# Kernel optimization log

Measured on AMD Instinct MI355X. Metric: run time of the kernel, lower is better.

The kernel has to match this reference:

```python
import jax, jax.numpy as jnp
import numpy as np

H = 8  # hidden size (hardcoded in the module)


def _lstm_scan(x, Wih, Whh, b):
    """Unidirectional LSTM over x:[B,T,I] with PyTorch gate order (i,f,g,o).
    Wih:[4H,I], Whh:[4H,H], b:[4H] (= b_ih + b_hh). Returns h seq [B,T,H]."""
    B = x.shape[0]
    # Precompute input projections for all timesteps in one GEMM: [T,B,4H]
    xg = jnp.einsum('bti,gi->tbg', x, Wih) + b

    def step(carry, xt):
        h, c = carry
        z = xt + h @ Whh.T
        i, f, g, o = jnp.split(z, 4, axis=-1)
        c = jax.nn.sigmoid(f) * c + jax.nn.sigmoid(i) * jnp.tanh(g)
        h = jax.nn.sigmoid(o) * jnp.tanh(c)
        return (h, c), h

    init = (jnp.zeros((B, H), x.dtype), jnp.zeros((B, H), x.dtype))
    _, hs = jax.lax.scan(step, init, xg)  # hs: [T,B,H]
    return jnp.swapaxes(hs, 0, 1)


def _bilstm(x, Wih_f, Whh_f, b_f, Wih_b, Whh_b, b_b):
    fwd = _lstm_scan(x, Wih_f, Whh_f, b_f)
    bwd = _lstm_scan(x[:, ::-1], Wih_b, Whh_b, b_b)[:, ::-1]
    return jnp.concatenate([fwd, bwd], axis=-1)  # [B,T,2H]


def setup_inputs() -> dict:
    key = jax.random.key(0)
    ks = jax.random.split(key, 17)
    s = 1.0 / np.sqrt(H)  # PyTorch uniform(-1/sqrt(H), 1/sqrt(H)) init

    def u(k, shape):
        return jax.random.uniform(k, shape, jnp.float32, -s, s)

    x = jax.random.normal(ks[0], (256, 4096, 8), jnp.float32)
    inp = {'x': x}
    # LSTM params: biases are b_ih + b_hh fused (mathematically identical)
    names = [('Wih1f', (4 * H, 8)), ('Whh1f', (4 * H, H)), ('b1f', (4 * H,)),
             ('Wih1b', (4 * H, 8)), ('Whh1b', (4 * H, H)), ('b1b', (4 * H,)),
             ('Wih2f', (4 * H, 8)), ('Whh2f', (4 * H, H)), ('b2f', (4 * H,)),
             ('Wih2b', (4 * H, 8)), ('Whh2b', (4 * H, H)), ('b2b', (4 * H,)),
             ('W1', (8, 2 * H)), ('bl1', (8,)),
             ('W2', (8, 2 * H)), ('bl2', (8,))]
    for i, (name, shape) in enumerate(names):
        inp[name] = u(ks[i + 1], shape)
    return inp


def reference(x, Wih1f, Whh1f, b1f, Wih1b, Whh1b, b1b,
              Wih2f, Whh2f, b2f, Wih2b, Whh2b, b2b,
              W1, bl1, W2, bl2):
    h1 = _bilstm(x, Wih1f, Whh1f, b1f, Wih1b, Whh1b, b1b)   # [B,T,16]
    y1 = h1 @ W1.T + bl1                                     # [B,T,8]
    h2 = _bilstm(y1, Wih2f, Whh2f, b2f, Wih2b, Whh2b, b2b)  # [B,T,16]
    return h2 @ W2.T + bl2                                   # [B,T,8]
```

## Files before the change

kernel.cpp:

```cpp
#include <hip/hip_runtime.h>

#define T_LEN 4096
#define B_SZ  256

typedef float v2f __attribute__((ext_vector_type(2)));
typedef float v4f __attribute__((ext_vector_type(4)));

__device__ __forceinline__ float fexp2(float x) { return __builtin_amdgcn_exp2f(x); }
__device__ __forceinline__ float frcp(float x)  { return __builtin_amdgcn_rcpf(x); }

template<int S>
__device__ __forceinline__ float rorN(float v) {
    return __int_as_float(__builtin_amdgcn_update_dpp(
        0, __float_as_int(v), 0x120 + S, 0xf, 0xf, true));
}

template<int OFF>
__device__ __forceinline__ v4f aload(const float* p) {
    v4f r;
    asm volatile("global_load_dwordx4 %0, %1, off offset:%2"
                 : "=v"(r) : "v"(p), "i"(OFF) : "memory");
    return r;
}
__device__ __forceinline__ void aatomic(float* p, float v) {
    asm volatile("global_atomic_add_f32 %0, %1, off"
                 :: "v"(p), "v"(v) : "memory");
}

__global__ void init_bias_kernel(const float* __restrict__ bl1,
                                 const float* __restrict__ bl2,
                                 float* __restrict__ y1,
                                 float* __restrict__ out)
{
    const long idx = (long)blockIdx.x * blockDim.x + threadIdx.x;
    float4 a1 = make_float4(bl1[0], bl1[1], bl1[2], bl1[3]);
    float4 b1 = make_float4(bl1[4], bl1[5], bl1[6], bl1[7]);
    float4 a2 = make_float4(bl2[0], bl2[1], bl2[2], bl2[3]);
    float4 b2 = make_float4(bl2[4], bl2[5], bl2[6], bl2[7]);
    float4* y4 = (float4*)y1;
    float4* o4 = (float4*)out;
    y4[idx * 2 + 0] = a1;
    y4[idx * 2 + 1] = b1;
    o4[idx * 2 + 0] = a2;
    o4[idx * 2 + 1] = b2;
}

template<int ST>
__device__ __forceinline__ void rec_body(
    const float* x,
    const float* Wih,
    const float* Whh,
    const float* bias,
    const float* Wp,
    int dcol,
    float* y,
    int b0)
{
    const int tid  = threadIdx.x;
    const int cl   = tid & 15;
    const int j    = cl & 7;
    const int half = cl >> 3;
    const int b    = b0 + (tid >> 4);

    const int rA = half * 16 + j;
    const int rB = half * 16 + 8 + j;

    const float NL2E = -1.4426950408889634f;
    const float GSC  = 2.0f * NL2E;
    const float sA   = half ? GSC : NL2E;
    const float sB   = NL2E;
    const float aselA = half ? 2.0f : 1.0f;
    const float bselA = half ? -1.0f : 0.0f;

    v2f Whk[8], Wik[8];
    float Wcp[8];
    #pragma unroll
    for (int s = 0; s < 8; ++s) {
        const int k = (j - s) & 7;
        Whk[s] = (v2f){Whh[rA * 8 + k] * sA, Whh[rB * 8 + k] * sB};
        Wcp[s] = Wp[j * 16 + dcol + k] * 0.5f;
    }
    #pragma unroll
    for (int k = 0; k < 8; ++k)
        Wik[k] = (v2f){Wih[rA * 8 + k] * sA, Wih[rB * 8 + k] * sB};
    const v2f bpk = (v2f){bias[rA] * sA, bias[rB] * sB};

    const int start = (ST > 0) ? 0 : (T_LEN - 1);
    const float* xp = x + ((long)b * T_LEN + start) * 8;
    float*       wp = y + ((long)b * T_LEN + start) * 8 + j;

    float c = 0.0f, h = 0.0f;

    auto step = [&](v4f xa, v4f xb, bool doProj) {
        v2f ip = bpk;
        ip = __builtin_elementwise_fma(Wik[0], (v2f){xa.x, xa.x}, ip);
        ip = __builtin_elementwise_fma(Wik[1], (v2f){xa.y, xa.y}, ip);
        ip = __builtin_elementwise_fma(Wik[2], (v2f){xa.z, xa.z}, ip);
        ip = __builtin_elementwise_fma(Wik[3], (v2f){xa.w, xa.w}, ip);
        ip = __builtin_elementwise_fma(Wik[4], (v2f){xb.x, xb.x}, ip);
        ip = __builtin_elementwise_fma(Wik[5], (v2f){xb.y, xb.y}, ip);
        ip = __builtin_elementwise_fma(Wik[6], (v2f){xb.z, xb.z}, ip);
        ip = __builtin_elementwise_fma(Wik[7], (v2f){xb.w, xb.w}, ip);

        float hr0 = h;
        float hr1 = rorN<1>(h);
        float hr2 = rorN<2>(h);
        float hr3 = rorN<3>(h);
        float hr4 = rorN<4>(h);
        float hr5 = rorN<5>(h);
        float hr6 = rorN<6>(h);
        float hr7 = rorN<7>(h);

        v2f a0 = ip, a1 = {0.0f, 0.0f};
        a0 = __builtin_elementwise_fma(Whk[0], (v2f){hr0, hr0}, a0);
        a1 = __builtin_elementwise_fma(Whk[1], (v2f){hr1, hr1}, a1);
        a0 = __builtin_elementwise_fma(Whk[2], (v2f){hr2, hr2}, a0);
        a1 = __builtin_elementwise_fma(Whk[3], (v2f){hr3, hr3}, a1);
        a0 = __builtin_elementwise_fma(Whk[4], (v2f){hr4, hr4}, a0);
        a1 = __builtin_elementwise_fma(Whk[5], (v2f){hr5, hr5}, a1);
        a0 = __builtin_elementwise_fma(Whk[6], (v2f){hr6, hr6}, a0);
        a1 = __builtin_elementwise_fma(Whk[7], (v2f){hr7, hr7}, a1);
        const v2f z = a0 + a1;

        if (doProj) {
            float pa = hr0 * Wcp[0];
            pa = fmaf(hr1, Wcp[1], pa);
            pa = fmaf(hr2, Wcp[2], pa);
            pa = fmaf(hr3, Wcp[3], pa);
            pa = fmaf(hr4, Wcp[4], pa);
            pa = fmaf(hr5, Wcp[5], pa);
            pa = fmaf(hr6, Wcp[6], pa);
            pa = fmaf(hr7, Wcp[7], pa);
            aatomic(wp, pa);
            wp += ST * 8;
        }

        const float vA = fmaf(frcp(1.0f + fexp2(z.x)), aselA, bselA);
        const float vB = frcp(1.0f + fexp2(z.y));

        const float pAx = rorN<8>(vA);
        const float pBx = rorN<8>(vB);
        const float gi = half ? pAx : vA;
        const float gf = half ? pBx : vB;
        const float gg = half ? vA  : pAx;
        const float go = half ? vB  : pBx;

        c = fmaf(gf, c, gi * gg);
        const float th = fmaf(frcp(1.0f + fexp2(c * GSC)), 2.0f, -1.0f);
        h = go * th;
    };

    v4f A0, A1, A2, A3, A4, A5, A6, A7;
    v4f B0, B1, B2, B3, B4, B5, B6, B7;
    v4f C0, C1, C2, C3, C4, C5, C6, C7;

#define AREGS A0, A1, A2, A3, A4, A5, A6, A7
#define BREGS B0, B1, B2, B3, B4, B5, B6, B7
#define CREGS C0, C1, C2, C3, C4, C5, C6, C7

#define LOADM_I(P0, P1, P2, P3, P4, P5, P6, P7)                                \
    P0 = aload<0>(xp);            P1 = aload<16>(xp);                          \
    P2 = aload<ST * 32>(xp);      P3 = aload<ST * 32 + 16>(xp);                \
    P4 = aload<ST * 64>(xp);      P5 = aload<ST * 64 + 16>(xp);                \
    P6 = aload<ST * 96>(xp);      P7 = aload<ST * 96 + 16>(xp);                \
    xp += ST * 32;
#define LOADM(REGS) LOADM_I(REGS)

#define WAITM_I(N, P0, P1, P2, P3, P4, P5, P6, P7)                             \
    asm volatile("s_waitcnt vmcnt(" #N ")"                                     \
        : "+v"(P0), "+v"(P1), "+v"(P2), "+v"(P3),                              \
          "+v"(P4), "+v"(P5), "+v"(P6), "+v"(P7) :: "memory")
#define WAITM(N, REGS) WAITM_I(N, REGS)

#define MACRO4_I(P0, P1, P2, P3, P4, P5, P6, P7, FIRSTPROJ)                    \
    step(P0, P1, FIRSTPROJ);                                                   \
    step(P2, P3, true);                                                        \
    step(P4, P5, true);                                                        \
    step(P6, P7, true);
#define MACRO4(REGS, FIRSTPROJ) MACRO4_I(REGS, FIRSTPROJ)

    asm volatile("s_waitcnt vmcnt(0)" ::: "memory");

    LOADM(AREGS)
    LOADM(BREGS)
    LOADM(CREGS)
    WAITM(16, AREGS); MACRO4(AREGS, false)
    LOADM(AREGS)
    WAITM(19, BREGS); MACRO4(BREGS, true)
    LOADM(BREGS)
    WAITM(23, CREGS); MACRO4(CREGS, true)

    for (int i = 0; i < 339; ++i) {
        LOADM(CREGS) WAITM(24, AREGS); MACRO4(AREGS, true)
        LOADM(AREGS) WAITM(24, BREGS); MACRO4(BREGS, true)
        LOADM(BREGS) WAITM(24, CREGS); MACRO4(CREGS, true)
    }
    LOADM(CREGS)
    WAITM(24, AREGS); MACRO4(AREGS, true)
    LOADM(AREGS)
    WAITM(24, BREGS); MACRO4(BREGS, true)
    WAITM(16, CREGS); MACRO4(CREGS, true)
    WAITM(8,  AREGS); MACRO4(AREGS, true)

#undef LOADM
#undef LOADM_I
#undef MACRO4
#undef MACRO4_I
#undef WAITM
#undef WAITM_I
#undef AREGS
#undef BREGS
#undef CREGS

    {
        float pa = h * Wcp[0];
        pa = fmaf(rorN<1>(h), Wcp[1], pa);
        pa = fmaf(rorN<2>(h), Wcp[2], pa);
        pa = fmaf(rorN<3>(h), Wcp[3], pa);
        pa = fmaf(rorN<4>(h), Wcp[4], pa);
        pa = fmaf(rorN<5>(h), Wcp[5], pa);
        pa = fmaf(rorN<6>(h), Wcp[6], pa);
        pa = fmaf(rorN<7>(h), Wcp[7], pa);
        aatomic(wp, pa);
    }
}

__global__ __launch_bounds__(64, 1)
void lstm_rec_kernel(const float* __restrict__ x,
                     const float* __restrict__ WihF, const float* __restrict__ WhhF,
                     const float* __restrict__ bF,
                     const float* __restrict__ WihB, const float* __restrict__ WhhB,
                     const float* __restrict__ bB,
                     const float* __restrict__ Wp,
                     float* __restrict__ y)
{
    if (blockIdx.x < 64)
        rec_body<1 >(x, WihF, WhhF, bF, Wp, 0, y, 4 * (int)blockIdx.x);
    else
        rec_body<-1>(x, WihB, WhhB, bB, Wp, 8, y, 4 * ((int)blockIdx.x - 64));
}

extern "C" void kernel_launch(void* const* d_in, const int* in_sizes, int n_in,
                              void* d_out, int out_size, void* d_ws, size_t ws_size,
                              hipStream_t stream)
{
    const float* x     = (const float*)d_in[0];
    const float* Wih1f = (const float*)d_in[1];
    const float* Whh1f = (const float*)d_in[2];
    const float* b1f   = (const float*)d_in[3];
    const float* Wih1b = (const float*)d_in[4];
    const float* Whh1b = (const float*)d_in[5];
    const float* b1b   = (const float*)d_in[6];
    const float* Wih2f = (const float*)d_in[7];
    const float* Whh2f = (const float*)d_in[8];
    const float* b2f   = (const float*)d_in[9];
    const float* Wih2b = (const float*)d_in[10];
    const float* Whh2b = (const float*)d_in[11];
    const float* b2b   = (const float*)d_in[12];
    const float* W1    = (const float*)d_in[13];
    const float* bl1   = (const float*)d_in[14];
    const float* W2    = (const float*)d_in[15];
    const float* bl2   = (const float*)d_in[16];

    float* out = (float*)d_out;
    float* y1  = (float*)d_ws;

    const int BT = B_SZ * T_LEN;

    init_bias_kernel<<<BT / 256, 256, 0, stream>>>(bl1, bl2, y1, out);

    lstm_rec_kernel<<<128, 64, 0, stream>>>(x, Wih1f, Whh1f, b1f,
                                            Wih1b, Whh1b, b1b, W1, y1);

    lstm_rec_kernel<<<128, 64, 0, stream>>>(y1, Wih2f, Whh2f, b2f,
                                            Wih2b, Whh2b, b2b, W2, out);
}
```

Measured before the change: 1.099 ms.

## Interleave two independent batch recurrences per thread group to hide latency

Each 16-lane group now carries two batch sequences (P and Q) and alternates their LSTM steps, so the dependent chain of one sequence can overlap with the other's. The grid is halved to 64 blocks, and the load pipeline and loop count are restructured to match. This is meant to hide the serial latency of the recurrence (DPP rotates, exp, rcp) through instruction-level parallelism. In exchange it uses fewer CUs and more registers per thread.

```diff
diff --git a/kernel.cpp b/kernel.cpp
--- a/kernel.cpp
+++ b/kernel.cpp
@@ -60,7 +60,8 @@
     const int cl   = tid & 15;
     const int j    = cl & 7;
     const int half = cl >> 3;
-    const int b    = b0 + (tid >> 4);
+    const int bP   = b0 + 2 * (tid >> 4);
+    const int bQ   = bP + 1;
 
     const int rA = half * 16 + j;
     const int rB = half * 16 + 8 + j;
@@ -86,12 +87,15 @@
     const v2f bpk = (v2f){bias[rA] * sA, bias[rB] * sB};
 
     const int start = (ST > 0) ? 0 : (T_LEN - 1);
-    const float* xp = x + ((long)b * T_LEN + start) * 8;
-    float*       wp = y + ((long)b * T_LEN + start) * 8 + j;
-
-    float c = 0.0f, h = 0.0f;
-
-    auto step = [&](v4f xa, v4f xb, bool doProj) {
+    const float* xpP = x + ((long)bP * T_LEN + start) * 8;
+    const float* xpQ = x + ((long)bQ * T_LEN + start) * 8;
+    float*       wpP = y + ((long)bP * T_LEN + start) * 8 + j;
+    float*       wpQ = y + ((long)bQ * T_LEN + start) * 8 + j;
+
+    float cP = 0.0f, hP = 0.0f, cQ = 0.0f, hQ = 0.0f;
+
+    auto step = [&](v4f xa, v4f xb, float& c, float& h, float*& wp,
+                    bool doProj) {
         v2f ip = bpk;
         ip = __builtin_elementwise_fma(Wik[0], (v2f){xa.x, xa.x}, ip);
         ip = __builtin_elementwise_fma(Wik[1], (v2f){xa.y, xa.y}, ip);
@@ -158,70 +162,75 @@
 #define BREGS B0, B1, B2, B3, B4, B5, B6, B7
 #define CREGS C0, C1, C2, C3, C4, C5, C6, C7
 
-#define LOADM_I(P0, P1, P2, P3, P4, P5, P6, P7)                                \
-    P0 = aload<0>(xp);            P1 = aload<16>(xp);                          \
-    P2 = aload<ST * 32>(xp);      P3 = aload<ST * 32 + 16>(xp);                \
-    P4 = aload<ST * 64>(xp);      P5 = aload<ST * 64 + 16>(xp);                \
-    P6 = aload<ST * 96>(xp);      P7 = aload<ST * 96 + 16>(xp);                \
-    xp += ST * 32;
-#define LOADM(REGS) LOADM_I(REGS)
-
-#define WAITM_I(N, P0, P1, P2, P3, P4, P5, P6, P7)                             \
+#define LOADG_I(P0, P1, P2, P3, P4, P5, P6, P7)                                \
+    P0 = aload<0>(xpP);       P1 = aload<16>(xpP);                             \
+    P2 = aload<ST * 32>(xpP); P3 = aload<ST * 32 + 16>(xpP);                   \
+    P4 = aload<0>(xpQ);       P5 = aload<16>(xpQ);                             \
+    P6 = aload<ST * 32>(xpQ); P7 = aload<ST * 32 + 16>(xpQ);                   \
+    xpP += ST * 16;           xpQ += ST * 16;
+#define LOADG(REGS) LOADG_I(REGS)
+
+#define WAITG_I(N, P0, P1, P2, P3, P4, P5, P6, P7)                             \
     asm volatile("s_waitcnt vmcnt(" #N ")"                                     \
         : "+v"(P0), "+v"(P1), "+v"(P2), "+v"(P3),                              \
           "+v"(P4), "+v"(P5), "+v"(P6), "+v"(P7) :: "memory")
-#define WAITM(N, REGS) WAITM_I(N, REGS)
-
-#define MACRO4_I(P0, P1, P2, P3, P4, P5, P6, P7, FIRSTPROJ)                    \
-    step(P0, P1, FIRSTPROJ);                                                   \
-    step(P2, P3, true);                                                        \
-    step(P4, P5, true);                                                        \
-    step(P6, P7, true);
-#define MACRO4(REGS, FIRSTPROJ) MACRO4_I(REGS, FIRSTPROJ)
+#define WAITG(N, REGS) WAITG_I(N, REGS)
+
+#define GROUP2_I(P0, P1, P2, P3, P4, P5, P6, P7, FIRSTPROJ)                    \
+    step(P0, P1, cP, hP, wpP, FIRSTPROJ);                                      \
+    step(P4, P5, cQ, hQ, wpQ, FIRSTPROJ);                                      \
+    step(P2, P3, cP, hP, wpP, true);                                           \
+    step(P6, P7, cQ, hQ, wpQ, true);
+#define GROUP2(REGS, FIRSTPROJ) GROUP2_I(REGS, FIRSTPROJ)
 
     asm volatile("s_waitcnt vmcnt(0)" ::: "memory");
 
-    LOADM(AREGS)
-    LOADM(BREGS)
-    LOADM(CREGS)
-    WAITM(16, AREGS); MACRO4(AREGS, false)
-    LOADM(AREGS)
-    WAITM(19, BREGS); MACRO4(BREGS, true)
-    LOADM(BREGS)
-    WAITM(23, CREGS); MACRO4(CREGS, true)
-
-    for (int i = 0; i < 339; ++i) {
-        LOADM(CREGS) WAITM(24, AREGS); MACRO4(AREGS, true)
-        LOADM(AREGS) WAITM(24, BREGS); MACRO4(BREGS, true)
-        LOADM(BREGS) WAITM(24, CREGS); MACRO4(CREGS, true)
+    LOADG(AREGS)
+    LOADG(BREGS)
+    LOADG(CREGS)
+    WAITG(16, AREGS); GROUP2(AREGS, false)
+    LOADG(AREGS)
+    WAITG(18, BREGS); GROUP2(BREGS, true)
+    LOADG(BREGS)
+    WAITG(22, CREGS); GROUP2(CREGS, true)
+
+    for (int i = 0; i < 681; ++i) {
+        LOADG(CREGS) WAITG(24, AREGS); GROUP2(AREGS, true)
+        LOADG(AREGS) WAITG(24, BREGS); GROUP2(BREGS, true)
+        LOADG(BREGS) WAITG(24, CREGS); GROUP2(CREGS, true)
     }
-    LOADM(CREGS)
-    WAITM(24, AREGS); MACRO4(AREGS, true)
-    LOADM(AREGS)
-    WAITM(24, BREGS); MACRO4(BREGS, true)
-    WAITM(16, CREGS); MACRO4(CREGS, true)
-    WAITM(8,  AREGS); MACRO4(AREGS, true)
-
-#undef LOADM
-#undef LOADM_I
-#undef MACRO4
-#undef MACRO4_I
-#undef WAITM
-#undef WAITM_I
+    WAITG(16, AREGS); GROUP2(AREGS, true)
+    WAITG(8,  BREGS); GROUP2(BREGS, true)
+
+#undef LOADG
+#undef LOADG_I
+#undef GROUP2
+#undef GROUP2_I
+#undef WAITG
+#undef WAITG_I
 #undef AREGS
 #undef BREGS
 #undef CREGS
 
     {
-        float pa = h * Wcp[0];
-        pa = fmaf(rorN<1>(h), Wcp[1], pa);
-        pa = fmaf(rorN<2>(h), Wcp[2], pa);
-        pa = fmaf(rorN<3>(h), Wcp[3], pa);
-        pa = fmaf(rorN<4>(h), Wcp[4], pa);
-        pa = fmaf(rorN<5>(h), Wcp[5], pa);
-        pa = fmaf(rorN<6>(h), Wcp[6], pa);
-        pa = fmaf(rorN<7>(h), Wcp[7], pa);
-        aatomic(wp, pa);
+        float pa = hP * Wcp[0];
+        pa = fmaf(rorN<1>(hP), Wcp[1], pa);
+        pa = fmaf(rorN<2>(hP), Wcp[2], pa);
+        pa = fmaf(rorN<3>(hP), Wcp[3], pa);
+        pa = fmaf(rorN<4>(hP), Wcp[4], pa);
+        pa = fmaf(rorN<5>(hP), Wcp[5], pa);
+        pa = fmaf(rorN<6>(hP), Wcp[6], pa);
+        pa = fmaf(rorN<7>(hP), Wcp[7], pa);
+        aatomic(wpP, pa);
+        float qa = hQ * Wcp[0];
+        qa = fmaf(rorN<1>(hQ), Wcp[1], qa);
+        qa = fmaf(rorN<2>(hQ), Wcp[2], qa);
+        qa = fmaf(rorN<3>(hQ), Wcp[3], qa);
+        qa = fmaf(rorN<4>(hQ), Wcp[4], qa);
+        qa = fmaf(rorN<5>(hQ), Wcp[5], qa);
+        qa = fmaf(rorN<6>(hQ), Wcp[6], qa);
+        qa = fmaf(rorN<7>(hQ), Wcp[7], qa);
+        aatomic(wpQ, qa);
     }
 }
 
@@ -234,10 +243,10 @@
                      const float* __restrict__ Wp,
                      float* __restrict__ y)
 {
-    if (blockIdx.x < 64)
-        rec_body<1 >(x, WihF, WhhF, bF, Wp, 0, y, 4 * (int)blockIdx.x);
+    if (blockIdx.x < 32)
+        rec_body<1 >(x, WihF, WhhF, bF, Wp, 0, y, 8 * (int)blockIdx.x);
     else
-        rec_body<-1>(x, WihB, WhhB, bB, Wp, 8, y, 4 * ((int)blockIdx.x - 64));
+        rec_body<-1>(x, WihB, WhhB, bB, Wp, 8, y, 8 * ((int)blockIdx.x - 32));
 }
 
 extern "C" void kernel_launch(void* const* d_in, const int* in_sizes, int n_in,
@@ -269,9 +278,9 @@
 
     init_bias_kernel<<<BT / 256, 256, 0, stream>>>(bl1, bl2, y1, out);
 
-    lstm_rec_kernel<<<128, 64, 0, stream>>>(x, Wih1f, Whh1f, b1f,
-                                            Wih1b, Whh1b, b1b, W1, y1);
-
-    lstm_rec_kernel<<<128, 64, 0, stream>>>(y1, Wih2f, Whh2f, b2f,
-                                            Wih2b, Whh2b, b2b, W2, out);
-}
+    lstm_rec_kernel<<<64, 64, 0, stream>>>(x, Wih1f, Whh1f, b1f,
+                                           Wih1b, Whh1b, b1b, W1, y1);
+
+    lstm_rec_kernel<<<64, 64, 0, stream>>>(y1, Wih2f, Whh2f, b2f,
+                                           Wih2b, Whh2b, b2b, W2, out);
+}
```

After: 2.052 ms. 1.87x slower.
